# Kernel optimization log

Measured on AMD Instinct MI355X. Metric: run time of the kernel, lower is better.

Reference implementation:

```python
import jax, jax.numpy as jnp
import numpy as np

B, N = 16384, 1024


def _bit_reversal_indices(n):
    bits = int(np.log2(n))
    val = np.arange(n)
    src = np.zeros(n, dtype=np.int64)
    for _ in range(bits):
        src = (src << 1) | (val & 1)
        val = val >> 1
    return src  # src[k] = source pair for target pair k


def _inter_stage_indices(n, stage_idx):
    prev = 2 ** stage_idx
    kb = np.arange(n // 2)
    g = kb // prev
    kw = kb % prev
    half = (kw >= prev // 2).astype(np.int64)
    off = kw % (prev // 2)
    nb = prev // 2
    sE = (2 * g) * nb + off
    sO = (2 * g + 1) * nb + off
    perm = np.empty(n, dtype=np.int64)
    perm[2 * kb] = 2 * sE + half
    perm[2 * kb + 1] = 2 * sO + half
    return perm


def _final_unscramble_indices(n):
    k = np.arange(n // 2)
    perm = np.empty(n, dtype=np.int64)
    perm[k] = 2 * k
    perm[k + n // 2] = 2 * k + 1
    return perm


def _butterfly_weights(n, stage_idx):
    # grouped 1x1 conv weights -> (n//2, 4, 4): out = W[g] @ in per group
    Nb = 2 ** (stage_idx + 1)
    nub = Nb // 2
    reps = n // Nb
    k = np.arange(nub)
    rW = np.cos(2.0 * np.pi * k / Nb)      # Re(W_Nb^k)
    iW = -np.sin(2.0 * np.pi * k / Nb)     # Im(W_Nb^k) (forward DFT twiddle)
    W = np.zeros((nub, 4, 4), dtype=np.float32)
    W[:, 0, 0] = 1.0; W[:, 0, 2] = rW;  W[:, 0, 3] = -iW
    W[:, 1, 1] = 1.0; W[:, 1, 2] = iW;  W[:, 1, 3] = rW
    W[:, 2, 0] = 1.0; W[:, 2, 2] = -rW; W[:, 2, 3] = iW
    W[:, 3, 1] = 1.0; W[:, 3, 2] = -iW; W[:, 3, 3] = -rW
    return np.tile(W, (reps, 1, 1))  # (n//2, 4, 4)


def setup_inputs() -> dict:
    key = jax.random.key(0)
    x = jax.random.normal(key, (B, 2 * N, 1, 1), dtype=jnp.float32)
    return {"x": x}


def reference(x) -> jnp.ndarray:
    b = x.shape[0]
    n = x.shape[1] // 2
    stages = int(np.log2(n))
    # pairs view: (B, N, 2) = interleaved [Re, Im]
    v = x.reshape(b, n, 2)
    v = v[:, jnp.asarray(_bit_reversal_indices(n)), :]
    for s in range(stages):
        if s > 0:
            v = v[:, jnp.asarray(_inter_stage_indices(n, s)), :]
        W = jnp.asarray(_butterfly_weights(n, s))       # (N/2, 4, 4)
        g = v.reshape(b, n // 2, 4)                     # 4 channels per group
        g = jnp.einsum('goi,bgi->bgo', W, g)            # grouped 1x1 conv
        v = g.reshape(b, n, 2)
    v = v[:, jnp.asarray(_final_unscramble_indices(n)), :]
    return v.reshape(b, 2 * n, 1, 1)
```

## Files before the change

kernel.cpp:

```cpp
#include <hip/hip_runtime.h>

#define NFFT 1024
#define TPB 256

__device__ __forceinline__ float2 cmul(float2 a, float2 b) {
  return make_float2(fmaf(a.x, b.x, -a.y * b.y), fmaf(a.x, b.y, a.y * b.x));
}
__device__ __forceinline__ float2 cadd(float2 a, float2 b) { return make_float2(a.x + b.x, a.y + b.y); }
__device__ __forceinline__ float2 csub(float2 a, float2 b) { return make_float2(a.x - b.x, a.y - b.y); }

__device__ __forceinline__ void dft4(const float2 v[4], float2 y[4]) {
  float2 s02 = cadd(v[0], v[2]), d02 = csub(v[0], v[2]);
  float2 s13 = cadd(v[1], v[3]), d13 = csub(v[1], v[3]);
  y[0] = cadd(s02, s13);
  y[2] = csub(s02, s13);
  y[1] = make_float2(d02.x + d13.y, d02.y - d13.x);
  y[3] = make_float2(d02.x - d13.y, d02.y + d13.x);
}

__device__ __forceinline__ float dpp_xor2(float x) {
  return __int_as_float(__builtin_amdgcn_update_dpp(0, __float_as_int(x), 0x4E, 0xF, 0xF, true));
}
__device__ __forceinline__ float dpp_xor1(float x) {
  return __int_as_float(__builtin_amdgcn_update_dpp(0, __float_as_int(x), 0xB1, 0xF, 0xF, true));
}

__device__ __forceinline__ void fft16(float2 z[16]) {
  float2 g[16];
  #pragma unroll
  for (int c0 = 0; c0 < 4; ++c0) {
    float2 v[4] = {z[c0], z[c0 + 4], z[c0 + 8], z[c0 + 12]};
    float2 y[4];
    dft4(v, y);
    g[4 * c0 + 0] = y[0]; g[4 * c0 + 1] = y[1]; g[4 * c0 + 2] = y[2]; g[4 * c0 + 3] = y[3];
  }
  const float C1 = 0.92387953251128674f, S1 = 0.38268343236508978f, R = 0.70710678118654752f;
  g[5]  = cmul(g[5],  make_float2( C1, -S1));
  g[6]  = cmul(g[6],  make_float2(  R,  -R));
  g[7]  = cmul(g[7],  make_float2( S1, -C1));
  g[9]  = cmul(g[9],  make_float2(  R,  -R));
  g[10] = make_float2(g[10].y, -g[10].x);
  g[11] = cmul(g[11], make_float2( -R,  -R));
  g[13] = cmul(g[13], make_float2( S1, -C1));
  g[14] = cmul(g[14], make_float2( -R,  -R));
  g[15] = cmul(g[15], make_float2(-C1,  S1));
  #pragma unroll
  for (int k0 = 0; k0 < 4; ++k0) {
    float2 v[4] = {g[k0], g[4 + k0], g[8 + k0], g[12 + k0]};
    float2 y[4];
    dft4(v, y);
    z[4 * k0 + 0] = y[0]; z[4 * k0 + 1] = y[1]; z[4 * k0 + 2] = y[2]; z[4 * k0 + 3] = y[3];
  }
}

__device__ __forceinline__ void twiddle_apply(float2 z[16], float2 u) {
  float2 w = u;
  #pragma unroll
  for (int k = 1; k < 16; ++k) {
    const int s = ((k & 3) << 2) | (k >> 2);
    z[s] = cmul(z[s], w);
    w = cmul(w, u);
  }
}

__global__ __launch_bounds__(TPB, 4) void fft1024_kernel(const float* __restrict__ in,
                                                         float* __restrict__ out,
                                                         int nrows) {
  __shared__ float2 lds[TPB / 64][NFFT];
  const int wv = threadIdx.x >> 6;
  const int lane = threadIdx.x & 63;
  const int row = blockIdx.x * (TPB / 64) + wv;
  if (row >= nrows) return;

  const float2* __restrict__ xin = reinterpret_cast<const float2*>(in) + (size_t)row * NFFT;
  float2* __restrict__ xout = reinterpret_cast<float2*>(out) + (size_t)row * NFFT;

  float2 z[16];
  #pragma unroll
  for (int c = 0; c < 16; ++c) z[c] = xin[lane + 64 * c];

  fft16(z);

  float sn, cs;
  __sincosf((float)lane * (-6.2831853071795864769f / 1024.0f), &sn, &cs);
  twiddle_apply(z, make_float2(cs, sn));

  {
    float2* buf = lds[wv];
    const int m = lane >> 2, p = lane & 3;
    #pragma unroll
    for (int s = 0; s < 16; ++s) {
      const int kap = (s >> 2) | ((s & 3) << 2);
      buf[m * 64 + ((p + 4 * kap) ^ m)] = z[s];
    }
    asm volatile("s_waitcnt lgkmcnt(0)" ::: "memory");
    __builtin_amdgcn_sched_barrier(0);
    #pragma unroll
    for (int mm = 0; mm < 16; ++mm) z[mm] = buf[mm * 64 + (lane ^ mm)];
  }

  fft16(z);

  const int p = lane & 3;
  __sincosf((float)p * (-6.2831853071795864769f / 64.0f), &sn, &cs);
  twiddle_apply(z, make_float2(cs, sn));

  const float sgn1 = (lane & 2) ? -1.0f : 1.0f;
  const float sgn2 = (lane & 1) ? -1.0f : 1.0f;
  const bool tw3 = ((lane & 3) == 3);
  #pragma unroll
  for (int s = 0; s < 16; ++s) {
    float px = dpp_xor2(z[s].x), py = dpp_xor2(z[s].y);
    float ax = fmaf(sgn1, z[s].x, px), ay = fmaf(sgn1, z[s].y, py);
    float bx = tw3 ? ay : ax;
    float by = tw3 ? -ax : ay;
    float qx = dpp_xor1(bx), qy = dpp_xor1(by);
    z[s].x = fmaf(sgn2, bx, qx);
    z[s].y = fmaf(sgn2, by, qy);
  }

  const int kap = lane >> 2;
  const int ur = ((p & 1) << 1) | (p >> 1);
  float2* __restrict__ orow = xout + kap + 256 * ur;
  #pragma unroll
  for (int s = 0; s < 16; ++s) {
    const int t = (s >> 2) | ((s & 3) << 2);
    orow[16 * t] = z[s];
  }
}

extern "C" void kernel_launch(void* const* d_in, const int* in_sizes, int n_in,
                              void* d_out, int out_size, void* d_ws, size_t ws_size,
                              hipStream_t stream) {
  const float* x = (const float*)d_in[0];
  float* out = (float*)d_out;
  const int rows = in_sizes[0] / (2 * NFFT);
  const int rpb = TPB / 64;
  const int blocks = (rows + rpb - 1) / rpb;
  fft1024_kernel<<<blocks, TPB, 0, stream>>>(x, out, rows);
}
```

Before: 230.4 us.

## Halve LDS per wave with two-phase transpose and raise occupancy target

The per-wave LDS transpose buffer drops from 1024 to 512 float2 entries. The exchange now runs in two phases: lanes 0-31 write and all lanes read rows 0-7, then lanes 32-63 write and all lanes read rows 8-15. The XOR swizzle changes to match. Launch bounds rise from 4 to 6 blocks per CU to take advantage of the smaller LDS footprint, at the cost of extra waits and half-idle writes during the transpose and tighter register limits, which could cause spills.

```diff
diff --git a/kernel.cpp b/kernel.cpp
--- a/kernel.cpp
+++ b/kernel.cpp
@@ -63,10 +63,10 @@
   }
 }
 
-__global__ __launch_bounds__(TPB, 4) void fft1024_kernel(const float* __restrict__ in,
+__global__ __launch_bounds__(TPB, 6) void fft1024_kernel(const float* __restrict__ in,
                                                          float* __restrict__ out,
                                                          int nrows) {
-  __shared__ float2 lds[TPB / 64][NFFT];
+  __shared__ float2 lds[TPB / 64][NFFT / 2];
   const int wv = threadIdx.x >> 6;
   const int lane = threadIdx.x & 63;
   const int row = blockIdx.x * (TPB / 64) + wv;
@@ -80,43 +80,61 @@
   for (int c = 0; c < 16; ++c) z[c] = xin[lane + 64 * c];
 
   fft16(z);
-
   float sn, cs;
   __sincosf((float)lane * (-6.2831853071795864769f / 1024.0f), &sn, &cs);
   twiddle_apply(z, make_float2(cs, sn));
 
+  float2 t2[16];
   {
     float2* buf = lds[wv];
     const int m = lane >> 2, p = lane & 3;
-    #pragma unroll
-    for (int s = 0; s < 16; ++s) {
-      const int kap = (s >> 2) | ((s & 3) << 2);
-      buf[m * 64 + ((p + 4 * kap) ^ m)] = z[s];
+
+    if (lane < 32) {
+      #pragma unroll
+      for (int s = 0; s < 16; ++s) {
+        const int kap = (s >> 2) | ((s & 3) << 2);
+        buf[(m & 7) * 64 + ((p + 4 * kap) ^ ((m & 3) << 2))] = z[s];
+      }
     }
     asm volatile("s_waitcnt lgkmcnt(0)" ::: "memory");
     __builtin_amdgcn_sched_barrier(0);
     #pragma unroll
-    for (int mm = 0; mm < 16; ++mm) z[mm] = buf[mm * 64 + (lane ^ mm)];
+    for (int mm = 0; mm < 8; ++mm)
+      t2[mm] = buf[mm * 64 + (lane ^ ((mm & 3) << 2))];
+    asm volatile("s_waitcnt lgkmcnt(0)" ::: "memory");
+    __builtin_amdgcn_sched_barrier(0);
+
+    if (lane >= 32) {
+      #pragma unroll
+      for (int s = 0; s < 16; ++s) {
+        const int kap = (s >> 2) | ((s & 3) << 2);
+        buf[(m & 7) * 64 + ((p + 4 * kap) ^ ((m & 3) << 2))] = z[s];
+      }
+    }
+    asm volatile("s_waitcnt lgkmcnt(0)" ::: "memory");
+    __builtin_amdgcn_sched_barrier(0);
+    #pragma unroll
+    for (int mm = 8; mm < 16; ++mm)
+      t2[mm] = buf[(mm & 7) * 64 + (lane ^ ((mm & 3) << 2))];
   }
 
-  fft16(z);
-
+  fft16(t2);
   const int p = lane & 3;
   __sincosf((float)p * (-6.2831853071795864769f / 64.0f), &sn, &cs);
-  twiddle_apply(z, make_float2(cs, sn));
+  twiddle_apply(t2, make_float2(cs, sn));
 
   const float sgn1 = (lane & 2) ? -1.0f : 1.0f;
   const float sgn2 = (lane & 1) ? -1.0f : 1.0f;
   const bool tw3 = ((lane & 3) == 3);
   #pragma unroll
   for (int s = 0; s < 16; ++s) {
-    float px = dpp_xor2(z[s].x), py = dpp_xor2(z[s].y);
-    float ax = fmaf(sgn1, z[s].x, px), ay = fmaf(sgn1, z[s].y, py);
+    float px = dpp_xor2(t2[s].x), py = dpp_xor2(t2[s].y);
+    float ax = fmaf(sgn1, t2[s].x, px), ay = fmaf(sgn1, t2[s].y, py);
     float bx = tw3 ? ay : ax;
     float by = tw3 ? -ax : ay;
     float qx = dpp_xor1(bx), qy = dpp_xor1(by);
-    z[s].x = fmaf(sgn2, bx, qx);
-    z[s].y = fmaf(sgn2, by, qy);
+    t2[s].x = fmaf(sgn2, bx, qx);
+    t2[s].y = fmaf(sgn2, by, qy);
   }
 
   const int kap = lane >> 2;
@@ -125,7 +143,7 @@
   #pragma unroll
   for (int s = 0; s < 16; ++s) {
     const int t = (s >> 2) | ((s & 3) << 2);
-    orow[16 * t] = z[s];
+    orow[16 * t] = t2[s];
   }
 }
 
```

Result: no change. 232.8 us (+1.0%).

## Process four rows per wave with double-buffered loads and nontemporal stores

Applied to the files above, without the earlier changes.

Each wave now handles four FFT rows and prefetches the next row into a second register array while the current row is computed, so global load latency is hidden. The two sincos twiddle bases are computed once per wave and reused across the four rows. The LDS swizzle is changed to XOR with (m&3)<<2, and output stores become nontemporal. In exchange, register pressure rises and the grid has a quarter as many blocks, which can lower occupancy. There is no bounds check for rows after the first, so the row count must be a multiple of four.

```diff
diff --git a/kernel.cpp b/kernel.cpp
--- a/kernel.cpp
+++ b/kernel.cpp
@@ -2,6 +2,7 @@
 
 #define NFFT 1024
 #define TPB 256
+#define ROWS 4
 
 __device__ __forceinline__ float2 cmul(float2 a, float2 b) {
   return make_float2(fmaf(a.x, b.x, -a.y * b.y), fmaf(a.x, b.y, a.y * b.x));
@@ -63,47 +64,30 @@
   }
 }
 
-__global__ __launch_bounds__(TPB, 4) void fft1024_kernel(const float* __restrict__ in,
-                                                         float* __restrict__ out,
-                                                         int nrows) {
-  __shared__ float2 lds[TPB / 64][NFFT];
-  const int wv = threadIdx.x >> 6;
-  const int lane = threadIdx.x & 63;
-  const int row = blockIdx.x * (TPB / 64) + wv;
-  if (row >= nrows) return;
+__device__ __forceinline__ void loadrow(float2 z[16], const float2* __restrict__ src, int lane) {
+  #pragma unroll
+  for (int c = 0; c < 16; ++c) z[c] = src[lane + 64 * c];
+}
 
-  const float2* __restrict__ xin = reinterpret_cast<const float2*>(in) + (size_t)row * NFFT;
-  float2* __restrict__ xout = reinterpret_cast<float2*>(out) + (size_t)row * NFFT;
+__device__ __forceinline__ void procrow(float2 z[16], float2* __restrict__ buf,
+                                        float2 u1, float2 u2, int lane,
+                                        float2* __restrict__ dst) {
+  fft16(z);
+  twiddle_apply(z, u1);
 
-  float2 z[16];
+  const int m = lane >> 2, p = lane & 3;
   #pragma unroll
-  for (int c = 0; c < 16; ++c) z[c] = xin[lane + 64 * c];
+  for (int s = 0; s < 16; ++s) {
+    const int kap = (s >> 2) | ((s & 3) << 2);
+    buf[m * 64 + ((p + 4 * kap) ^ ((m & 3) << 2))] = z[s];
+  }
+  asm volatile("s_waitcnt lgkmcnt(0)" ::: "memory");
+  __builtin_amdgcn_sched_barrier(0);
+  #pragma unroll
+  for (int mm = 0; mm < 16; ++mm) z[mm] = buf[mm * 64 + (lane ^ ((mm & 3) << 2))];
 
   fft16(z);
-
-  float sn, cs;
-  __sincosf((float)lane * (-6.2831853071795864769f / 1024.0f), &sn, &cs);
-  twiddle_apply(z, make_float2(cs, sn));
-
-  {
-    float2* buf = lds[wv];
-    const int m = lane >> 2, p = lane & 3;
-    #pragma unroll
-    for (int s = 0; s < 16; ++s) {
-      const int kap = (s >> 2) | ((s & 3) << 2);
-      buf[m * 64 + ((p + 4 * kap) ^ m)] = z[s];
-    }
-    asm volatile("s_waitcnt lgkmcnt(0)" ::: "memory");
-    __builtin_amdgcn_sched_barrier(0);
-    #pragma unroll
-    for (int mm = 0; mm < 16; ++mm) z[mm] = buf[mm * 64 + (lane ^ mm)];
-  }
-
-  fft16(z);
-
-  const int p = lane & 3;
-  __sincosf((float)p * (-6.2831853071795864769f / 64.0f), &sn, &cs);
-  twiddle_apply(z, make_float2(cs, sn));
+  twiddle_apply(z, u2);
 
   const float sgn1 = (lane & 2) ? -1.0f : 1.0f;
   const float sgn2 = (lane & 1) ? -1.0f : 1.0f;
@@ -121,12 +105,43 @@
 
   const int kap = lane >> 2;
   const int ur = ((p & 1) << 1) | (p >> 1);
-  float2* __restrict__ orow = xout + kap + 256 * ur;
+  float2* __restrict__ orow = dst + kap + 256 * ur;
   #pragma unroll
   for (int s = 0; s < 16; ++s) {
     const int t = (s >> 2) | ((s & 3) << 2);
-    orow[16 * t] = z[s];
+    __builtin_nontemporal_store(*reinterpret_cast<const double*>(&z[s]),
+                                reinterpret_cast<double*>(orow + 16 * t));
   }
+}
+
+__global__ __launch_bounds__(TPB, 4) void fft1024_kernel(const float* __restrict__ in,
+                                                         float* __restrict__ out,
+                                                         int nrows) {
+  __shared__ float2 lds[TPB / 64][NFFT];
+  const int wv = threadIdx.x >> 6;
+  const int lane = threadIdx.x & 63;
+  const int r0 = (blockIdx.x * (TPB / 64) + wv) * ROWS;
+  if (r0 >= nrows) return;
+
+  const float2* __restrict__ xin = reinterpret_cast<const float2*>(in) + (size_t)r0 * NFFT;
+  float2* __restrict__ xout = reinterpret_cast<float2*>(out) + (size_t)r0 * NFFT;
+  float2* buf = lds[wv];
+
+  float sn, cs;
+  __sincosf((float)lane * (-6.2831853071795864769f / 1024.0f), &sn, &cs);
+  const float2 u1 = make_float2(cs, sn);
+  __sincosf((float)(lane & 3) * (-6.2831853071795864769f / 64.0f), &sn, &cs);
+  const float2 u2 = make_float2(cs, sn);
+
+  float2 A[16], B[16];
+  loadrow(A, xin, lane);
+  loadrow(B, xin + NFFT, lane);
+  procrow(A, buf, u1, u2, lane, xout);
+  loadrow(A, xin + 2 * NFFT, lane);
+  procrow(B, buf, u1, u2, lane, xout + NFFT);
+  loadrow(B, xin + 3 * NFFT, lane);
+  procrow(A, buf, u1, u2, lane, xout + 2 * NFFT);
+  procrow(B, buf, u1, u2, lane, xout + 3 * NFFT);
 }
 
 extern "C" void kernel_launch(void* const* d_in, const int* in_sizes, int n_in,
@@ -135,7 +150,7 @@
   const float* x = (const float*)d_in[0];
   float* out = (float*)d_out;
   const int rows = in_sizes[0] / (2 * NFFT);
-  const int rpb = TPB / 64;
+  const int rpb = (TPB / 64) * ROWS;
   const int blocks = (rows + rpb - 1) / rpb;
   fft1024_kernel<<<blocks, TPB, 0, stream>>>(x, out, rows);
 }
```

After: 271.8 us. 1.18x slower.

## Stage global loads and stores through LDS with 16-byte vector accesses

Applied to the files above, without the earlier changes.

Global input is now read as float4 (two complex values per lane) into LDS, then redistributed to the per-lane layout. The output goes the same way: results are scattered into LDS with an XOR swizzle and written back as contiguous float4 stores, replacing the strided float2 global stores. The transpose swizzle also changes from XOR by row index to XOR by (row&3)<<2, aimed at fewer LDS bank conflicts. The aim is wider, fully coalesced global transactions, at the cost of two extra LDS round trips and wait barriers per row.

```diff
diff --git a/kernel.cpp b/kernel.cpp
--- a/kernel.cpp
+++ b/kernel.cpp
@@ -66,42 +66,50 @@
 __global__ __launch_bounds__(TPB, 4) void fft1024_kernel(const float* __restrict__ in,
                                                          float* __restrict__ out,
                                                          int nrows) {
-  __shared__ float2 lds[TPB / 64][NFFT];
+  __shared__ __align__(16) float2 lds[TPB / 64][NFFT];
   const int wv = threadIdx.x >> 6;
   const int lane = threadIdx.x & 63;
   const int row = blockIdx.x * (TPB / 64) + wv;
   if (row >= nrows) return;
 
-  const float2* __restrict__ xin = reinterpret_cast<const float2*>(in) + (size_t)row * NFFT;
-  float2* __restrict__ xout = reinterpret_cast<float2*>(out) + (size_t)row * NFFT;
+  const float4* __restrict__ xin4 = reinterpret_cast<const float4*>(in) + (size_t)row * (NFFT / 2);
+  float4* __restrict__ xout4 = reinterpret_cast<float4*>(out) + (size_t)row * (NFFT / 2);
+  float2* buf = lds[wv];
+
+  float4 v4[8];
+  #pragma unroll
+  for (int j = 0; j < 8; ++j) v4[j] = xin4[lane + 64 * j];
+  #pragma unroll
+  for (int j = 0; j < 8; ++j)
+    *reinterpret_cast<float4*>(&buf[2 * lane + 128 * j]) = v4[j];
+  asm volatile("s_waitcnt lgkmcnt(0)" ::: "memory");
+  __builtin_amdgcn_sched_barrier(0);
 
   float2 z[16];
   #pragma unroll
-  for (int c = 0; c < 16; ++c) z[c] = xin[lane + 64 * c];
+  for (int c = 0; c < 16; ++c) z[c] = buf[lane + 64 * c];
+  asm volatile("s_waitcnt lgkmcnt(0)" ::: "memory");
+  __builtin_amdgcn_sched_barrier(0);
 
   fft16(z);
-
   float sn, cs;
   __sincosf((float)lane * (-6.2831853071795864769f / 1024.0f), &sn, &cs);
   twiddle_apply(z, make_float2(cs, sn));
 
-  {
-    float2* buf = lds[wv];
-    const int m = lane >> 2, p = lane & 3;
-    #pragma unroll
-    for (int s = 0; s < 16; ++s) {
-      const int kap = (s >> 2) | ((s & 3) << 2);
-      buf[m * 64 + ((p + 4 * kap) ^ m)] = z[s];
-    }
-    asm volatile("s_waitcnt lgkmcnt(0)" ::: "memory");
-    __builtin_amdgcn_sched_barrier(0);
-    #pragma unroll
-    for (int mm = 0; mm < 16; ++mm) z[mm] = buf[mm * 64 + (lane ^ mm)];
+  const int m = lane >> 2, p = lane & 3;
+  #pragma unroll
+  for (int s = 0; s < 16; ++s) {
+    const int kap = (s >> 2) | ((s & 3) << 2);
+    buf[m * 64 + ((p + 4 * kap) ^ ((m & 3) << 2))] = z[s];
   }
+  asm volatile("s_waitcnt lgkmcnt(0)" ::: "memory");
+  __builtin_amdgcn_sched_barrier(0);
+  #pragma unroll
+  for (int mm = 0; mm < 16; ++mm) z[mm] = buf[mm * 64 + (lane ^ ((mm & 3) << 2))];
+  asm volatile("s_waitcnt lgkmcnt(0)" ::: "memory");
+  __builtin_amdgcn_sched_barrier(0);
 
   fft16(z);
-
-  const int p = lane & 3;
   __sincosf((float)p * (-6.2831853071795864769f / 64.0f), &sn, &cs);
   twiddle_apply(z, make_float2(cs, sn));
 
@@ -121,11 +129,19 @@
 
   const int kap = lane >> 2;
   const int ur = ((p & 1) << 1) | (p >> 1);
-  float2* __restrict__ orow = xout + kap + 256 * ur;
+  const int x16 = ur << 4;
   #pragma unroll
   for (int s = 0; s < 16; ++s) {
     const int t = (s >> 2) | ((s & 3) << 2);
-    orow[16 * t] = z[s];
+    const int idx = kap + 16 * t + 256 * ur;
+    buf[idx ^ x16] = z[s];
+  }
+  asm volatile("s_waitcnt lgkmcnt(0)" ::: "memory");
+  __builtin_amdgcn_sched_barrier(0);
+  #pragma unroll
+  for (int j = 0; j < 8; ++j) {
+    float4 w = *reinterpret_cast<const float4*>(&buf[(2 * lane + 128 * j) ^ ((j >> 1) << 4)]);
+    xout4[lane + 64 * j] = w;
   }
 }
 
```

Measured after the change: 229.4 us. Within noise of the previous version (-0.4%).
